# Performance work log

Hardware: AMD Instinct MI355X
Metric: run time of the kernel (lower is better)

Reference implementation:

```python
import jax, jax.numpy as jnp
import numpy as np

N = 32768       # total nodes = NUM_GRAPHS * T
F_IN = 32       # num_features
HC = 64         # hidden_channels
HEADS = 4
E = 524288      # edges before self-loops
NUM_GRAPHS = 64 # == batch.max()+1 by construction
T = 512         # time steps per graph (N // NUM_GRAPHS)
OUT = 24        # output_size
NEG_SLOPE = 0.2 # PyG GATConv default


def gat_layer(x, src, dst, W, a_src, a_dst, b, n_nodes):
    """PyG GATConv (concat=True) with edge softmax over incoming edges."""
    H, C = a_src.shape
    h = (x @ W).reshape(n_nodes, H, C)                    # [N,H,C]
    alpha_src = jnp.sum(h * a_src, axis=-1)               # [N,H]
    alpha_dst = jnp.sum(h * a_dst, axis=-1)               # [N,H]
    e = jax.nn.leaky_relu(alpha_src[src] + alpha_dst[dst], NEG_SLOPE)  # [E,H]
    m = jax.ops.segment_max(e, dst, num_segments=n_nodes)
    e = jnp.exp(e - m[dst])
    s = jax.ops.segment_sum(e, dst, num_segments=n_nodes)
    alpha = e / (s[dst] + 1e-16)                          # [E,H]
    msg = h[src] * alpha[..., None]                       # [E,H,C]
    out = jax.ops.segment_sum(msg, dst, num_segments=n_nodes)  # [N,H,C]
    return out.reshape(n_nodes, H * C) + b


def gru_layer(x, Wih, Whh, bih, bhh):
    """torch nn.GRU single layer, batch_first input x: [B,T,Hin] -> ([B,T,H], h_T)."""
    Bsz = x.shape[0]
    H = Whh.shape[1]

    def step(h, xt):
        gi = xt @ Wih.T + bih
        gh = h @ Whh.T + bhh
        ir, iz, inn = jnp.split(gi, 3, axis=-1)
        hr, hz, hn = jnp.split(gh, 3, axis=-1)
        r = jax.nn.sigmoid(ir + hr)
        z = jax.nn.sigmoid(iz + hz)
        n = jnp.tanh(inn + r * hn)
        h_new = (1.0 - z) * n + z * h
        return h_new, h_new

    h0 = jnp.zeros((Bsz, H), x.dtype)
    hT, ys = jax.lax.scan(step, h0, jnp.swapaxes(x, 0, 1))
    return jnp.swapaxes(ys, 0, 1), hT


def setup_inputs() -> dict:
    key = jax.random.key(0)
    ks = jax.random.split(key, 24)
    sc = 0.1
    inp = {
        "x": jax.random.normal(ks[0], (N, F_IN), dtype=jnp.float32),
        "edge_index": jax.random.randint(ks[1], (2, E), 0, N, dtype=jnp.int32),
        "batch": jnp.repeat(jnp.arange(NUM_GRAPHS, dtype=jnp.int32), T),
        # GAT layer 1: F_IN -> HC x HEADS (concat)
        "W1": sc * jax.random.normal(ks[2], (F_IN, HEADS * HC), dtype=jnp.float32),
        "a_src1": sc * jax.random.normal(ks[3], (HEADS, HC), dtype=jnp.float32),
        "a_dst1": sc * jax.random.normal(ks[4], (HEADS, HC), dtype=jnp.float32),
        "b1": jnp.zeros((HEADS * HC,), dtype=jnp.float32),
        # GAT layer 2: HEADS*HC -> HC, 1 head
        "W2": sc * jax.random.normal(ks[5], (HEADS * HC, HC), dtype=jnp.float32),
        "a_src2": sc * jax.random.normal(ks[6], (1, HC), dtype=jnp.float32),
        "a_dst2": sc * jax.random.normal(ks[7], (1, HC), dtype=jnp.float32),
        "b2": jnp.zeros((HC,), dtype=jnp.float32),
        # GRU (2 layers, input_size == hidden_size == HC)
        "gru_Wih0": sc * jax.random.normal(ks[8], (3 * HC, HC), dtype=jnp.float32),
        "gru_Whh0": sc * jax.random.normal(ks[9], (3 * HC, HC), dtype=jnp.float32),
        "gru_bih0": jnp.zeros((3 * HC,), dtype=jnp.float32),
        "gru_bhh0": jnp.zeros((3 * HC,), dtype=jnp.float32),
        "gru_Wih1": sc * jax.random.normal(ks[10], (3 * HC, HC), dtype=jnp.float32),
        "gru_Whh1": sc * jax.random.normal(ks[11], (3 * HC, HC), dtype=jnp.float32),
        "gru_bih1": jnp.zeros((3 * HC,), dtype=jnp.float32),
        "gru_bhh1": jnp.zeros((3 * HC,), dtype=jnp.float32),
        # Linear head
        "Wl": sc * jax.random.normal(ks[12], (OUT, HC), dtype=jnp.float32),
        "bl": jnp.zeros((OUT,), dtype=jnp.float32),
    }
    return inp


def reference(x, edge_index, batch, W1, a_src1, a_dst1, b1, W2, a_src2, a_dst2, b2,
              gru_Wih0, gru_Whh0, gru_bih0, gru_bhh0,
              gru_Wih1, gru_Whh1, gru_bih1, gru_bhh1, Wl, bl):
    # PyG GATConv default add_self_loops=True
    loops = jnp.arange(N, dtype=edge_index.dtype)
    src = jnp.concatenate([edge_index[0], loops])
    dst = jnp.concatenate([edge_index[1], loops])

    h = jax.nn.elu(gat_layer(x, src, dst, W1, a_src1, a_dst1, b1, N))   # [N, HEADS*HC]
    h = jax.nn.elu(gat_layer(h, src, dst, W2, a_src2, a_dst2, b2, N))   # [N, HC]

    # batch is repeat(arange(NUM_GRAPHS), T) so batch.max()+1 == NUM_GRAPHS (static)
    seq = h.reshape(NUM_GRAPHS, T, HC)
    seq, _ = gru_layer(seq, gru_Wih0, gru_Whh0, gru_bih0, gru_bhh0)
    _, hT = gru_layer(seq, gru_Wih1, gru_Whh1, gru_bih1, gru_bhh1)      # [B, HC]
    return hT @ Wl.T + bl                                               # [B, OUT]
```

## Files before the change

kernel.cpp:

```cpp
#include <hip/hip_runtime.h>
#include <hip/hip_bf16.h>

#define N_NODES 32768
#define F_IN    32
#define HC      64
#define HEADS   4
#define NE      524288
#define NET     (NE + N_NODES)
#define NG      64
#define TT      512
#define OUTF    24

__device__ __forceinline__ float lrelu(float x){ return x > 0.f ? x : 0.2f*x; }
__device__ __forceinline__ float eluf (float x){ return x > 0.f ? x : __expf(x)-1.f; }
__device__ __forceinline__ float sigmf(float x){ return 1.f/(1.f+__expf(-x)); }
__device__ __forceinline__ float tanhfast(float x){ return 1.f - 2.f/(__expf(2.f*x)+1.f); }

__global__ __launch_bounds__(256) void k_deg(const int* __restrict__ ei,
                                             int* __restrict__ deg){
  int e = blockIdx.x*256 + threadIdx.x;
  int d = (e < NE) ? ei[NE+e] : (e - NE);
  atomicAdd(deg + d, 1);
}

__global__ __launch_bounds__(1024) void k_scan(const int* __restrict__ deg,
                                               int* __restrict__ rowptr){
  __shared__ int ps[1024];
  const int t = threadIdx.x;
  const int base = t*32;
  int local[32]; int s = 0;
  #pragma unroll
  for(int i=0;i<32;i++){ local[i]=deg[base+i]; s+=local[i]; }
  ps[t]=s; __syncthreads();
  for(int off=1; off<1024; off<<=1){
    int v = (t>=off) ? ps[t-off] : 0;
    __syncthreads();
    ps[t]+=v;
    __syncthreads();
  }
  int run = (t==0) ? 0 : ps[t-1];
  #pragma unroll
  for(int i=0;i<32;i++){ rowptr[base+i]=run; run+=local[i]; }
  if(t==1023) rowptr[N_NODES]=run;
}

__global__ __launch_bounds__(256) void k_fill(const int* __restrict__ ei,
                                              const int* __restrict__ rowptr,
                                              int* __restrict__ cur,
                                              int* __restrict__ col){
  int e = blockIdx.x*256 + threadIdx.x;
  int s, d;
  if(e < NE){ s = ei[e]; d = ei[NE+e]; } else { s = e-NE; d = s; }
  int pos = atomicAdd(cur + d, 1);
  col[rowptr[d] + pos] = s;
}

__global__ __launch_bounds__(256) void k_gemm1(const float* __restrict__ x,
                                               const float* __restrict__ W1,
                                               float* __restrict__ h1){
  __shared__ __align__(16) float xs[64*32];
  __shared__ __align__(16) float ws[32*256];
  const int tid = threadIdx.x;
  const int row0 = blockIdx.x*64;
  const float4* xg = (const float4*)(x + row0*F_IN);
  float4* xs4 = (float4*)xs;
  for(int i=tid;i<512;i+=256) xs4[i]=xg[i];
  const float4* wg=(const float4*)W1; float4* ws4=(float4*)ws;
  for(int i=tid;i<2048;i+=256) ws4[i]=wg[i];
  __syncthreads();
  float wc[32];
  #pragma unroll
  for(int k=0;k<32;k++) wc[k]=ws[k*256+tid];
  for(int r=0;r<64;r++){
    const float4* xr=(const float4*)(xs + r*32);
    float acc=0.f;
    #pragma unroll
    for(int k4=0;k4<8;k4++){
      float4 v=xr[k4];
      acc += v.x*wc[4*k4]+v.y*wc[4*k4+1]+v.z*wc[4*k4+2]+v.w*wc[4*k4+3];
    }
    h1[(row0+r)*256+tid]=acc;
  }
}

__global__ __launch_bounds__(256) void k_alpha1(const float* __restrict__ h1,
                                                const float* __restrict__ a_src,
                                                const float* __restrict__ a_dst,
                                                float* __restrict__ as1,
                                                float* __restrict__ ad1){
  int t = blockIdx.x*256 + threadIdx.x;
  int n = t>>2, h = t&3;
  const float4* hp=(const float4*)(h1 + n*256 + h*64);
  const float4* ap=(const float4*)(a_src + h*64);
  const float4* dp=(const float4*)(a_dst + h*64);
  float sa=0.f, sd=0.f;
  #pragma unroll
  for(int i=0;i<16;i++){
    float4 v=hp[i], a=ap[i], d=dp[i];
    sa += v.x*a.x+v.y*a.y+v.z*a.z+v.w*a.w;
    sd += v.x*d.x+v.y*d.y+v.z*d.z+v.w*d.w;
  }
  as1[t]=sa; ad1[t]=sd;
}

__global__ __launch_bounds__(256) void k_gat1(const int* __restrict__ rowptr,
                                              const int* __restrict__ col,
                                              const float* __restrict__ as1,
                                              const float* __restrict__ ad1,
                                              const float* __restrict__ h1,
                                              const float* __restrict__ b1,
                                              float* __restrict__ out1){
  const int node = blockIdx.x*4 + (threadIdx.x>>6);
  const int lane = threadIdx.x & 63;
  const int h    = lane>>4;
  const int beg = rowptr[node], end = rowptr[node+1];
  const float ad = ad1[node*4+h];
  float4 acc = make_float4(0.f,0.f,0.f,0.f);
  float s = 0.f;
  int j = beg;
  for(; j+1 < end; j += 2){
    int s0 = col[j], s1 = col[j+1];
    float w0 = __expf(lrelu(as1[s0*4+h] + ad));
    float w1 = __expf(lrelu(as1[s1*4+h] + ad));
    float4 v0 = *(const float4*)(h1 + s0*256 + lane*4);
    float4 v1 = *(const float4*)(h1 + s1*256 + lane*4);
    acc.x += w0*v0.x + w1*v1.x;
    acc.y += w0*v0.y + w1*v1.y;
    acc.z += w0*v0.z + w1*v1.z;
    acc.w += w0*v0.w + w1*v1.w;
    s += w0 + w1;
  }
  if(j < end){
    int s0 = col[j];
    float w0 = __expf(lrelu(as1[s0*4+h] + ad));
    float4 v0 = *(const float4*)(h1 + s0*256 + lane*4);
    acc.x += w0*v0.x; acc.y += w0*v0.y; acc.z += w0*v0.z; acc.w += w0*v0.w;
    s += w0;
  }
  const float inv = 1.f/(s + 1e-16f);
  float4 bb = ((const float4*)b1)[lane];
  float4 o;
  o.x = eluf(acc.x*inv + bb.x);
  o.y = eluf(acc.y*inv + bb.y);
  o.z = eluf(acc.z*inv + bb.z);
  o.w = eluf(acc.w*inv + bb.w);
  ((float4*)(out1 + node*256))[lane] = o;
}

__global__ __launch_bounds__(256) void k_gemm2(const float* __restrict__ in,
                                               const float* __restrict__ W2,
                                               float* __restrict__ h2){
  __shared__ __align__(16) float xs[64*256];
  const int tid=threadIdx.x;
  const int row0=blockIdx.x*64;
  const float4* xg=(const float4*)(in + row0*256);
  float4* xs4=(float4*)xs;
  for(int i=tid;i<4096;i+=256) xs4[i]=xg[i];
  __syncthreads();
  const int c0=(tid&15)*4;
  const int r0=(tid>>4)*4;
  float acc[4][4]={};
  for(int k=0;k<256;k+=4){
    float wv[4][4];
    #pragma unroll
    for(int i=0;i<4;i++){
      float4 w=*(const float4*)(W2+(k+i)*64+c0);
      wv[i][0]=w.x; wv[i][1]=w.y; wv[i][2]=w.z; wv[i][3]=w.w;
    }
    #pragma unroll
    for(int i=0;i<4;i++){
      float4 xv=*(const float4*)(xs+(r0+i)*256+k);
      #pragma unroll
      for(int j=0;j<4;j++)
        acc[i][j]+=xv.x*wv[0][j]+xv.y*wv[1][j]+xv.z*wv[2][j]+xv.w*wv[3][j];
    }
  }
  #pragma unroll
  for(int i=0;i<4;i++)
    *(float4*)(h2+(row0+r0+i)*64+c0)=make_float4(acc[i][0],acc[i][1],acc[i][2],acc[i][3]);
}

__global__ __launch_bounds__(256) void k_alpha2(const float* __restrict__ h2,
                                                const float* __restrict__ a_src,
                                                const float* __restrict__ a_dst,
                                                float* __restrict__ as2,
                                                float* __restrict__ ad2){
  int n = blockIdx.x*256 + threadIdx.x;
  const float4* hp=(const float4*)(h2+n*64);
  float sa=0.f, sd=0.f;
  #pragma unroll
  for(int i=0;i<16;i++){
    float4 v=hp[i];
    float4 a=((const float4*)a_src)[i];
    float4 d=((const float4*)a_dst)[i];
    sa+=v.x*a.x+v.y*a.y+v.z*a.z+v.w*a.w;
    sd+=v.x*d.x+v.y*d.y+v.z*d.z+v.w*d.w;
  }
  as2[n]=sa; ad2[n]=sd;
}

__global__ __launch_bounds__(256) void k_gat2(const int* __restrict__ rowptr,
                                              const int* __restrict__ col,
                                              const float* __restrict__ as2,
                                              const float* __restrict__ ad2,
                                              const float* __restrict__ h2,
                                              const float* __restrict__ b2,
                                              float* __restrict__ out2){
  const int node = blockIdx.x*4 + (threadIdx.x>>6);
  const int lane = threadIdx.x & 63;
  const int beg = rowptr[node], end = rowptr[node+1];
  const float ad = ad2[node];
  float acc = 0.f, s = 0.f;
  int j = beg;
  for(; j+1 < end; j += 2){
    int s0 = col[j], s1 = col[j+1];
    float w0 = __expf(lrelu(as2[s0] + ad));
    float w1 = __expf(lrelu(as2[s1] + ad));
    acc += w0*h2[s0*64+lane] + w1*h2[s1*64+lane];
    s += w0 + w1;
  }
  if(j < end){
    int s0 = col[j];
    float w0 = __expf(lrelu(as2[s0] + ad));
    acc += w0*h2[s0*64+lane];
    s += w0;
  }
  const float inv = 1.f/(s + 1e-16f);
  out2[node*64+lane] = eluf(acc*inv + b2[lane]);
}

__global__ __launch_bounds__(256) void k_gemm_gi(const float* __restrict__ in,
                                                 const float* __restrict__ Wih,
                                                 const float* __restrict__ bih,
                                                 float* __restrict__ gi){
  __shared__ __align__(16) float xs[64*64];
  __shared__ float wT[64*192];
  const int tid=threadIdx.x;
  const int row0=blockIdx.x*64;
  const float4* xg=(const float4*)(in+row0*64);
  float4* xs4=(float4*)xs;
  for(int i=tid;i<1024;i+=256) xs4[i]=xg[i];
  for(int i=tid;i<12288;i+=256){ wT[(i&63)*192+(i>>6)] = Wih[i]; }
  __syncthreads();
  if(tid<192){
    float wr[64];
    #pragma unroll
    for(int k=0;k<64;k++) wr[k]=wT[k*192+tid];
    const float bj=bih[tid];
    for(int r=0;r<64;r++){
      float acc=bj;
      const float4* xr=(const float4*)(xs+r*64);
      #pragma unroll
      for(int k4=0;k4<16;k4++){
        float4 v=xr[k4];
        acc+=v.x*wr[4*k4]+v.y*wr[4*k4+1]+v.z*wr[4*k4+2]+v.w*wr[4*k4+3];
      }
      gi[(row0+r)*192+tid]=acc;
    }
  }
}

__global__ __launch_bounds__(576) void k_gru2(const float* __restrict__ gi1,
                                              const float* __restrict__ Whh0,
                                              const float* __restrict__ bhh0,
                                              const float* __restrict__ Wih1,
                                              const float* __restrict__ bih1,
                                              const float* __restrict__ Whh1,
                                              const float* __restrict__ bhh1,
                                              const float* __restrict__ Wl,
                                              const float* __restrict__ bl,
                                              float* __restrict__ fout){
  __shared__ __align__(16) float h1s[64];
  __shared__ __align__(16) float h2s[64];
  __shared__ float gis1[192];
  __shared__ float gh1s[192];
  __shared__ float gi2s[192];
  __shared__ float gh2s[192];
  const int tid = threadIdx.x;
  const int b   = blockIdx.x;

  const float* Wsel; float bsel; int g;
  if(tid < 192){ g = tid;     Wsel = Whh0; bsel = bhh0[g]; }
  else if(tid < 384){ g = tid-192; Wsel = Wih1; bsel = bih1[g]; }
  else{ g = tid-384; Wsel = Whh1; bsel = bhh1[g]; }
  float wr[64];
  {
    const float4* wp = (const float4*)(Wsel + g*64);
    #pragma unroll
    for(int k4=0;k4<16;k4++){
      float4 w = wp[k4];
      wr[4*k4]=w.x; wr[4*k4+1]=w.y; wr[4*k4+2]=w.z; wr[4*k4+3]=w.w;
    }
  }
  if(tid < 64){ h1s[tid]=0.f; h2s[tid]=0.f; }
  __syncthreads();

  const float* gib = gi1 + (size_t)b*TT*192;
  float giv = (tid < 192) ? gib[tid] : 0.f;

  for(int i=0;i<=TT;i++){
    if(tid < 192){
      if(i < TT){
        gis1[tid] = giv;
        if(i+1 < TT) giv = gib[(i+1)*192 + tid];
        float a0=0.f,a1=0.f,a2=0.f,a3=0.f;
        #pragma unroll
        for(int k4=0;k4<16;k4++){
          float4 h4 = *(const float4*)(h1s + 4*k4);
          a0 += h4.x*wr[4*k4];   a1 += h4.y*wr[4*k4+1];
          a2 += h4.z*wr[4*k4+2]; a3 += h4.w*wr[4*k4+3];
        }
        gh1s[tid] = bsel + ((a0+a1)+(a2+a3));
      }
    } else if(tid < 384){
      if(i >= 1){
        float a0=0.f,a1=0.f,a2=0.f,a3=0.f;
        #pragma unroll
        for(int k4=0;k4<16;k4++){
          float4 h4 = *(const float4*)(h1s + 4*k4);
          a0 += h4.x*wr[4*k4];   a1 += h4.y*wr[4*k4+1];
          a2 += h4.z*wr[4*k4+2]; a3 += h4.w*wr[4*k4+3];
        }
        gi2s[g] = bsel + ((a0+a1)+(a2+a3));
      }
    } else {
      if(i >= 1){
        float a0=0.f,a1=0.f,a2=0.f,a3=0.f;
        #pragma unroll
        for(int k4=0;k4<16;k4++){
          float4 h4 = *(const float4*)(h2s + 4*k4);
          a0 += h4.x*wr[4*k4];   a1 += h4.y*wr[4*k4+1];
          a2 += h4.z*wr[4*k4+2]; a3 += h4.w*wr[4*k4+3];
        }
        gh2s[g] = bsel + ((a0+a1)+(a2+a3));
      }
    }
    __syncthreads();
    if(tid < 64){
      if(i < TT){
        float r = sigmf(gis1[tid]     + gh1s[tid]);
        float z = sigmf(gis1[64+tid]  + gh1s[64+tid]);
        float n = tanhfast(gis1[128+tid] + r*gh1s[128+tid]);
        h1s[tid] = (1.f-z)*n + z*h1s[tid];
      }
    } else if(tid < 128){
      if(i >= 1){
        int c = tid-64;
        float r = sigmf(gi2s[c]     + gh2s[c]);
        float z = sigmf(gi2s[64+c]  + gh2s[64+c]);
        float n = tanhfast(gi2s[128+c] + r*gh2s[128+c]);
        h2s[c] = (1.f-z)*n + z*h2s[c];
      }
    }
    __syncthreads();
  }

  if(tid < 24){
    float acc = bl[tid];
    const float4* wl4 = (const float4*)(Wl + tid*64);
    #pragma unroll
    for(int k4=0;k4<16;k4++){
      float4 h4 = *(const float4*)(h2s + 4*k4);
      float4 w4 = wl4[k4];
      acc += h4.x*w4.x + h4.y*w4.y + h4.z*w4.z + h4.w*w4.w;
    }
    fout[b*24+tid] = acc;
  }
}

extern "C" void kernel_launch(void* const* d_in, const int* in_sizes, int n_in,
                              void* d_out, int out_size, void* d_ws, size_t ws_size,
                              hipStream_t stream){
  const float* x     =(const float*)d_in[0];
  const int*   ei    =(const int*  )d_in[1];
  const float* W1    =(const float*)d_in[3];
  const float* a_src1=(const float*)d_in[4];
  const float* a_dst1=(const float*)d_in[5];
  const float* b1    =(const float*)d_in[6];
  const float* W2    =(const float*)d_in[7];
  const float* a_src2=(const float*)d_in[8];
  const float* a_dst2=(const float*)d_in[9];
  const float* b2    =(const float*)d_in[10];
  const float* Wih0  =(const float*)d_in[11];
  const float* Whh0  =(const float*)d_in[12];
  const float* bih0  =(const float*)d_in[13];
  const float* bhh0  =(const float*)d_in[14];
  const float* Wih1  =(const float*)d_in[15];
  const float* Whh1  =(const float*)d_in[16];
  const float* bih1  =(const float*)d_in[17];
  const float* bhh1  =(const float*)d_in[18];
  const float* Wl    =(const float*)d_in[19];
  const float* bl    =(const float*)d_in[20];

  float* ws   = (float*)d_ws;
  float* h1   = ws;
  float* gi   = ws;
  float* out1 = ws + 8388608;
  float* out2 = out1;
  float* h2   = ws + 16777216;
  float* as1  = ws + 18874368;
  float* ad1  = as1 + 131072;
  float* as2  = ad1 + 131072;
  float* ad2  = as2 + 32768;
  int* rowptr = (int*)(ad2 + 32768);
  int* deg    = rowptr + 32800;
  int* cur    = deg + 32768;
  int* col    = cur + 32768;
  float* fo   = (float*)d_out;

  hipMemsetAsync(deg, 0, 2*32768*sizeof(int), stream);

  k_deg  <<<2176,256,0,stream>>>(ei,deg);
  k_scan <<<1  ,1024,0,stream>>>(deg,rowptr);
  k_fill <<<2176,256,0,stream>>>(ei,rowptr,cur,col);

  k_gemm1 <<<512 ,256,0,stream>>>(x,W1,h1);
  k_alpha1<<<512 ,256,0,stream>>>(h1,a_src1,a_dst1,as1,ad1);
  k_gat1  <<<8192,256,0,stream>>>(rowptr,col,as1,ad1,h1,b1,out1);
  k_gemm2 <<<512 ,256,0,stream>>>(out1,W2,h2);
  k_alpha2<<<128 ,256,0,stream>>>(h2,a_src2,a_dst2,as2,ad2);
  k_gat2  <<<8192,256,0,stream>>>(rowptr,col,as2,ad2,h2,b2,out2);
  k_gemm_gi<<<512,256,0,stream>>>(out2,Wih0,bih0,gi);
  k_gru2  <<<64 ,576,0,stream>>>(gi,Whh0,bhh0,Wih1,bih1,Whh1,bhh1,Wl,bl,fo);
  (void)in_sizes; (void)n_in; (void)out_size; (void)ws_size;
}
```

Before: 875.1 us.

## Restructure GRU kernel into wavefront-specialized pipeline with readlane broadcasts

Replaces the 576-thread two-barrier GRU kernel with a 256-thread kernel where each wavefront owns one role: layer-0 recurrence, layer-1 input projection, layer-1 recurrence, and a prefetcher for the gi stream. Each lane keeps three weight rows in registers and broadcasts the hidden state with readlane instead of reading it from shared memory, and the gate math is fused into the same wavefront. The stages are skewed by one step so each iteration needs only one barrier. The cost is much higher register pressure (192 weight floats per lane) and a two-step pipeline fill.

New measurement: 850.5 us. 1.03x faster.

```diff
diff --git a/kernel.cpp b/kernel.cpp
--- a/kernel.cpp
+++ b/kernel.cpp
@@ -15,6 +15,9 @@
 __device__ __forceinline__ float eluf (float x){ return x > 0.f ? x : __expf(x)-1.f; }
 __device__ __forceinline__ float sigmf(float x){ return 1.f/(1.f+__expf(-x)); }
 __device__ __forceinline__ float tanhfast(float x){ return 1.f - 2.f/(__expf(2.f*x)+1.f); }
+__device__ __forceinline__ float bcast(float v, int k){
+  return __int_as_float(__builtin_amdgcn_readlane(__float_as_int(v), k));
+}
 
 __global__ __launch_bounds__(256) void k_deg(const int* __restrict__ ei,
                                              int* __restrict__ deg){
@@ -260,107 +263,125 @@
   }
 }
 
-__global__ __launch_bounds__(576) void k_gru2(const float* __restrict__ gi1,
-                                              const float* __restrict__ Whh0,
-                                              const float* __restrict__ bhh0,
-                                              const float* __restrict__ Wih1,
-                                              const float* __restrict__ bih1,
-                                              const float* __restrict__ Whh1,
-                                              const float* __restrict__ bhh1,
-                                              const float* __restrict__ Wl,
-                                              const float* __restrict__ bl,
-                                              float* __restrict__ fout){
-  __shared__ __align__(16) float h1s[64];
-  __shared__ __align__(16) float h2s[64];
-  __shared__ float gis1[192];
-  __shared__ float gh1s[192];
-  __shared__ float gi2s[192];
-  __shared__ float gh2s[192];
-  const int tid = threadIdx.x;
-  const int b   = blockIdx.x;
-
-  const float* Wsel; float bsel; int g;
-  if(tid < 192){ g = tid;     Wsel = Whh0; bsel = bhh0[g]; }
-  else if(tid < 384){ g = tid-192; Wsel = Wih1; bsel = bih1[g]; }
-  else{ g = tid-384; Wsel = Whh1; bsel = bhh1[g]; }
-  float wr[64];
+__global__ __launch_bounds__(256,1) void k_gru_pipe(const float* __restrict__ gi1,
+                                                    const float* __restrict__ Whh0,
+                                                    const float* __restrict__ bhh0,
+                                                    const float* __restrict__ Wih1,
+                                                    const float* __restrict__ bih1,
+                                                    const float* __restrict__ Whh1,
+                                                    const float* __restrict__ bhh1,
+                                                    const float* __restrict__ Wl,
+                                                    const float* __restrict__ bl,
+                                                    float* __restrict__ fout){
+  __shared__ float h1s[2][64];
+  __shared__ float gi2s[2][192];
+  __shared__ float gi1b[4][192];
+  __shared__ float h2fin[64];
+  const int tid  = threadIdx.x;
+  const int w    = tid >> 6;
+  const int lane = tid & 63;
+  const int b    = blockIdx.x;
+  const float* gib = gi1 + (size_t)b*TT*192;
+
+  float w0[64], w1[64], w2[64];
+  float b0=0.f, b1=0.f, b2=0.f;
   {
-    const float4* wp = (const float4*)(Wsel + g*64);
-    #pragma unroll
-    for(int k4=0;k4<16;k4++){
-      float4 w = wp[k4];
-      wr[4*k4]=w.x; wr[4*k4+1]=w.y; wr[4*k4+2]=w.z; wr[4*k4+3]=w.w;
-    }
-  }
-  if(tid < 64){ h1s[tid]=0.f; h2s[tid]=0.f; }
+    const float* Wsel = (w==0)?Whh0 : (w==1)?Whh1 : Wih1;
+    const float* bsel = (w==0)?bhh0 : (w==1)?bhh1 : bih1;
+    if(w < 3){
+      const float4* r0 = (const float4*)(Wsel + lane*64);
+      const float4* r1 = (const float4*)(Wsel + (64+lane)*64);
+      const float4* r2 = (const float4*)(Wsel + (128+lane)*64);
+      #pragma unroll
+      for(int k4=0;k4<16;k4++){
+        float4 a=r0[k4], c=r1[k4], d=r2[k4];
+        w0[4*k4]=a.x; w0[4*k4+1]=a.y; w0[4*k4+2]=a.z; w0[4*k4+3]=a.w;
+        w1[4*k4]=c.x; w1[4*k4+1]=c.y; w1[4*k4+2]=c.z; w1[4*k4+3]=c.w;
+        w2[4*k4]=d.x; w2[4*k4+1]=d.y; w2[4*k4+2]=d.z; w2[4*k4+3]=d.w;
+      }
+      b0=bsel[lane]; b1=bsel[64+lane]; b2=bsel[128+lane];
+    } else {
+      #pragma unroll
+      for(int s=0;s<2;s++){
+        float v0=gib[s*192+lane], v1=gib[s*192+64+lane], v2=gib[s*192+128+lane];
+        gi1b[s][lane]=v0; gi1b[s][64+lane]=v1; gi1b[s][128+lane]=v2;
+      }
+    }
+  }
+  float h1r = 0.f, h2r = 0.f;
   __syncthreads();
 
-  const float* gib = gi1 + (size_t)b*TT*192;
-  float giv = (tid < 192) ? gib[tid] : 0.f;
-
-  for(int i=0;i<=TT;i++){
-    if(tid < 192){
+  for(int i=0;i<TT+2;i++){
+    if(w == 0){
       if(i < TT){
-        gis1[tid] = giv;
-        if(i+1 < TT) giv = gib[(i+1)*192 + tid];
-        float a0=0.f,a1=0.f,a2=0.f,a3=0.f;
+        float gr = gi1b[i&3][lane];
+        float gz = gi1b[i&3][64+lane];
+        float gn = gi1b[i&3][128+lane];
+        float a0=b0, a1=b1, a2=b2;
         #pragma unroll
-        for(int k4=0;k4<16;k4++){
-          float4 h4 = *(const float4*)(h1s + 4*k4);
-          a0 += h4.x*wr[4*k4];   a1 += h4.y*wr[4*k4+1];
-          a2 += h4.z*wr[4*k4+2]; a3 += h4.w*wr[4*k4+3];
+        for(int k=0;k<64;k++){
+          float hk = bcast(h1r, k);
+          a0 = fmaf(hk, w0[k], a0);
+          a1 = fmaf(hk, w1[k], a1);
+          a2 = fmaf(hk, w2[k], a2);
         }
-        gh1s[tid] = bsel + ((a0+a1)+(a2+a3));
-      }
-    } else if(tid < 384){
-      if(i >= 1){
-        float a0=0.f,a1=0.f,a2=0.f,a3=0.f;
+        float r = sigmf(gr + a0);
+        float z = sigmf(gz + a1);
+        float n = tanhfast(gn + r*a2);
+        h1r = (1.f-z)*n + z*h1r;
+        h1s[i&1][lane] = h1r;
+      }
+    } else if(w == 2){
+      if(i >= 1 && i <= TT){
+        float h1v = h1s[(i-1)&1][lane];
+        float a0=b0, a1=b1, a2=b2;
         #pragma unroll
-        for(int k4=0;k4<16;k4++){
-          float4 h4 = *(const float4*)(h1s + 4*k4);
-          a0 += h4.x*wr[4*k4];   a1 += h4.y*wr[4*k4+1];
-          a2 += h4.z*wr[4*k4+2]; a3 += h4.w*wr[4*k4+3];
+        for(int k=0;k<64;k++){
+          float hk = bcast(h1v, k);
+          a0 = fmaf(hk, w0[k], a0);
+          a1 = fmaf(hk, w1[k], a1);
+          a2 = fmaf(hk, w2[k], a2);
         }
-        gi2s[g] = bsel + ((a0+a1)+(a2+a3));
+        gi2s[(i-1)&1][lane]     = a0;
+        gi2s[(i-1)&1][64+lane]  = a1;
+        gi2s[(i-1)&1][128+lane] = a2;
+      }
+    } else if(w == 1){
+      if(i >= 2){
+        float gr = gi2s[i&1][lane];
+        float gz = gi2s[i&1][64+lane];
+        float gn = gi2s[i&1][128+lane];
+        float a0=b0, a1=b1, a2=b2;
+        #pragma unroll
+        for(int k=0;k<64;k++){
+          float hk = bcast(h2r, k);
+          a0 = fmaf(hk, w0[k], a0);
+          a1 = fmaf(hk, w1[k], a1);
+          a2 = fmaf(hk, w2[k], a2);
+        }
+        float r = sigmf(gr + a0);
+        float z = sigmf(gz + a1);
+        float n = tanhfast(gn + r*a2);
+        h2r = (1.f-z)*n + z*h2r;
       }
     } else {
-      if(i >= 1){
-        float a0=0.f,a1=0.f,a2=0.f,a3=0.f;
-        #pragma unroll
-        for(int k4=0;k4<16;k4++){
-          float4 h4 = *(const float4*)(h2s + 4*k4);
-          a0 += h4.x*wr[4*k4];   a1 += h4.y*wr[4*k4+1];
-          a2 += h4.z*wr[4*k4+2]; a3 += h4.w*wr[4*k4+3];
-        }
-        gh2s[g] = bsel + ((a0+a1)+(a2+a3));
+      int st = i+2;
+      if(st < TT){
+        float v0=gib[st*192+lane], v1=gib[st*192+64+lane], v2=gib[st*192+128+lane];
+        gi1b[st&3][lane]=v0; gi1b[st&3][64+lane]=v1; gi1b[st&3][128+lane]=v2;
       }
     }
     __syncthreads();
-    if(tid < 64){
-      if(i < TT){
-        float r = sigmf(gis1[tid]     + gh1s[tid]);
-        float z = sigmf(gis1[64+tid]  + gh1s[64+tid]);
-        float n = tanhfast(gis1[128+tid] + r*gh1s[128+tid]);
-        h1s[tid] = (1.f-z)*n + z*h1s[tid];
-      }
-    } else if(tid < 128){
-      if(i >= 1){
-        int c = tid-64;
-        float r = sigmf(gi2s[c]     + gh2s[c]);
-        float z = sigmf(gi2s[64+c]  + gh2s[64+c]);
-        float n = tanhfast(gi2s[128+c] + r*gh2s[128+c]);
-        h2s[c] = (1.f-z)*n + z*h2s[c];
-      }
-    }
-    __syncthreads();
-  }
-
+  }
+
+  if(w == 1) h2fin[lane] = h2r;
+  __syncthreads();
   if(tid < 24){
     float acc = bl[tid];
     const float4* wl4 = (const float4*)(Wl + tid*64);
     #pragma unroll
     for(int k4=0;k4<16;k4++){
-      float4 h4 = *(const float4*)(h2s + 4*k4);
+      float4 h4 = *(const float4*)(h2fin + 4*k4);
       float4 w4 = wl4[k4];
       acc += h4.x*w4.x + h4.y*w4.y + h4.z*w4.z + h4.w*w4.w;
     }
@@ -421,6 +442,6 @@
   k_alpha2<<<128 ,256,0,stream>>>(h2,a_src2,a_dst2,as2,ad2);
   k_gat2  <<<8192,256,0,stream>>>(rowptr,col,as2,ad2,h2,b2,out2);
   k_gemm_gi<<<512,256,0,stream>>>(out2,Wih0,bih0,gi);
-  k_gru2  <<<64 ,576,0,stream>>>(gi,Whh0,bhh0,Wih1,bih1,Whh1,bhh1,Wl,bl,fo);
+  k_gru_pipe<<<64,256,0,stream>>>(gi,Whh0,bhh0,Wih1,bih1,Whh1,bhh1,Wl,bl,fo);
   (void)in_sizes; (void)n_in; (void)out_size; (void)ws_size;
 }
```

## Restructure GRU kernel into wave crews with readlane broadcast and prefetch wave

Applied to the files above, without the earlier changes.

The fused two-layer GRU kernel is reorganised into ten 64-lane waves. Nine waves compute the three recurrent matvecs, taking h from a per-lane register broadcast via readlane instead of float4 LDS reads. A tenth wave double-buffers the next timestep's input gates into shared memory. The gate updates for the two layers are moved onto separate waves (9 and 7). This aims to shorten the serial per-step critical path in the latency-bound recurrence, at the cost of one extra wave and 64 serial readlane+FMA steps per matvec.

New measurement: 979.0 us. 11.9% more time.

```diff
diff --git a/kernel.cpp b/kernel.cpp
--- a/kernel.cpp
+++ b/kernel.cpp
@@ -15,6 +15,9 @@
 __device__ __forceinline__ float eluf (float x){ return x > 0.f ? x : __expf(x)-1.f; }
 __device__ __forceinline__ float sigmf(float x){ return 1.f/(1.f+__expf(-x)); }
 __device__ __forceinline__ float tanhfast(float x){ return 1.f - 2.f/(__expf(2.f*x)+1.f); }
+__device__ __forceinline__ float bcast(float v, int k){
+  return __int_as_float(__builtin_amdgcn_readlane(__float_as_int(v), k));
+}
 
 __global__ __launch_bounds__(256) void k_deg(const int* __restrict__ ei,
                                              int* __restrict__ deg){
@@ -260,96 +263,84 @@
   }
 }
 
-__global__ __launch_bounds__(576) void k_gru2(const float* __restrict__ gi1,
-                                              const float* __restrict__ Whh0,
-                                              const float* __restrict__ bhh0,
-                                              const float* __restrict__ Wih1,
-                                              const float* __restrict__ bih1,
-                                              const float* __restrict__ Whh1,
-                                              const float* __restrict__ bhh1,
-                                              const float* __restrict__ Wl,
-                                              const float* __restrict__ bl,
-                                              float* __restrict__ fout){
-  __shared__ __align__(16) float h1s[64];
-  __shared__ __align__(16) float h2s[64];
-  __shared__ float gis1[192];
+__global__ __launch_bounds__(640,1) void k_gru9(const float* __restrict__ gi1,
+                                                const float* __restrict__ Whh0,
+                                                const float* __restrict__ bhh0,
+                                                const float* __restrict__ Wih1,
+                                                const float* __restrict__ bih1,
+                                                const float* __restrict__ Whh1,
+                                                const float* __restrict__ bhh1,
+                                                const float* __restrict__ Wl,
+                                                const float* __restrict__ bl,
+                                                float* __restrict__ fout){
+  __shared__ float h1s[64];
+  __shared__ float h2s[64];
   __shared__ float gh1s[192];
   __shared__ float gi2s[192];
   __shared__ float gh2s[192];
-  const int tid = threadIdx.x;
-  const int b   = blockIdx.x;
-
-  const float* Wsel; float bsel; int g;
-  if(tid < 192){ g = tid;     Wsel = Whh0; bsel = bhh0[g]; }
-  else if(tid < 384){ g = tid-192; Wsel = Wih1; bsel = bih1[g]; }
-  else{ g = tid-384; Wsel = Whh1; bsel = bhh1[g]; }
+  __shared__ float g1r[2][192];
+  const int tid  = threadIdx.x;
+  const int w    = tid >> 6;
+  const int lane = tid & 63;
+  const int b    = blockIdx.x;
+  const float* gib = gi1 + (size_t)b*TT*192;
+
   float wr[64];
-  {
-    const float4* wp = (const float4*)(Wsel + g*64);
+  float bias = 0.f;
+  int   crew = 0, row = 0;
+  float* dst = gh1s;
+  if(w < 9){
+    crew = w / 3;
+    row  = (w % 3)*64 + lane;
+    const float* W  = (crew==0) ? Whh0 : (crew==1) ? Wih1 : Whh1;
+    const float* bb = (crew==0) ? bhh0 : (crew==1) ? bih1 : bhh1;
+    dst = (crew==0) ? gh1s : (crew==1) ? gi2s : gh2s;
+    const float4* wp = (const float4*)(W + row*64);
     #pragma unroll
     for(int k4=0;k4<16;k4++){
-      float4 w = wp[k4];
-      wr[4*k4]=w.x; wr[4*k4+1]=w.y; wr[4*k4+2]=w.z; wr[4*k4+3]=w.w;
-    }
+      float4 v = wp[k4];
+      wr[4*k4]=v.x; wr[4*k4+1]=v.y; wr[4*k4+2]=v.z; wr[4*k4+3]=v.w;
+    }
+    bias = bb[row];
+  } else {
+    g1r[0][lane]     = gib[lane];
+    g1r[0][64+lane]  = gib[64+lane];
+    g1r[0][128+lane] = gib[128+lane];
   }
   if(tid < 64){ h1s[tid]=0.f; h2s[tid]=0.f; }
   __syncthreads();
 
-  const float* gib = gi1 + (size_t)b*TT*192;
-  float giv = (tid < 192) ? gib[tid] : 0.f;
-
   for(int i=0;i<=TT;i++){
-    if(tid < 192){
-      if(i < TT){
-        gis1[tid] = giv;
-        if(i+1 < TT) giv = gib[(i+1)*192 + tid];
-        float a0=0.f,a1=0.f,a2=0.f,a3=0.f;
+    if(w < 9){
+      bool act = (crew==0) ? (i < TT) : (i >= 1);
+      if(act){
+        float hv = (crew==2) ? h2s[lane] : h1s[lane];
+        float acc = bias;
         #pragma unroll
-        for(int k4=0;k4<16;k4++){
-          float4 h4 = *(const float4*)(h1s + 4*k4);
-          a0 += h4.x*wr[4*k4];   a1 += h4.y*wr[4*k4+1];
-          a2 += h4.z*wr[4*k4+2]; a3 += h4.w*wr[4*k4+3];
-        }
-        gh1s[tid] = bsel + ((a0+a1)+(a2+a3));
-      }
-    } else if(tid < 384){
-      if(i >= 1){
-        float a0=0.f,a1=0.f,a2=0.f,a3=0.f;
-        #pragma unroll
-        for(int k4=0;k4<16;k4++){
-          float4 h4 = *(const float4*)(h1s + 4*k4);
-          a0 += h4.x*wr[4*k4];   a1 += h4.y*wr[4*k4+1];
-          a2 += h4.z*wr[4*k4+2]; a3 += h4.w*wr[4*k4+3];
-        }
-        gi2s[g] = bsel + ((a0+a1)+(a2+a3));
+        for(int k=0;k<64;k++) acc = fmaf(bcast(hv,k), wr[k], acc);
+        dst[row] = acc;
       }
     } else {
+      int st = i+1;
+      if(st < TT){
+        float v0=gib[st*192+lane], v1=gib[st*192+64+lane], v2=gib[st*192+128+lane];
+        g1r[st&1][lane]=v0; g1r[st&1][64+lane]=v1; g1r[st&1][128+lane]=v2;
+      }
+    }
+    __syncthreads();
+    if(w == 9){
+      if(i < TT){
+        float r = sigmf(g1r[i&1][lane]     + gh1s[lane]);
+        float z = sigmf(g1r[i&1][64+lane]  + gh1s[64+lane]);
+        float n = tanhfast(g1r[i&1][128+lane] + r*gh1s[128+lane]);
+        h1s[lane] = (1.f-z)*n + z*h1s[lane];
+      }
+    } else if(w == 7){
       if(i >= 1){
-        float a0=0.f,a1=0.f,a2=0.f,a3=0.f;
-        #pragma unroll
-        for(int k4=0;k4<16;k4++){
-          float4 h4 = *(const float4*)(h2s + 4*k4);
-          a0 += h4.x*wr[4*k4];   a1 += h4.y*wr[4*k4+1];
-          a2 += h4.z*wr[4*k4+2]; a3 += h4.w*wr[4*k4+3];
-        }
-        gh2s[g] = bsel + ((a0+a1)+(a2+a3));
-      }
-    }
-    __syncthreads();
-    if(tid < 64){
-      if(i < TT){
-        float r = sigmf(gis1[tid]     + gh1s[tid]);
-        float z = sigmf(gis1[64+tid]  + gh1s[64+tid]);
-        float n = tanhfast(gis1[128+tid] + r*gh1s[128+tid]);
-        h1s[tid] = (1.f-z)*n + z*h1s[tid];
-      }
-    } else if(tid < 128){
-      if(i >= 1){
-        int c = tid-64;
-        float r = sigmf(gi2s[c]     + gh2s[c]);
-        float z = sigmf(gi2s[64+c]  + gh2s[64+c]);
-        float n = tanhfast(gi2s[128+c] + r*gh2s[128+c]);
-        h2s[c] = (1.f-z)*n + z*h2s[c];
+        float r = sigmf(gi2s[lane]     + gh2s[lane]);
+        float z = sigmf(gi2s[64+lane]  + gh2s[64+lane]);
+        float n = tanhfast(gi2s[128+lane] + r*gh2s[128+lane]);
+        h2s[lane] = (1.f-z)*n + z*h2s[lane];
       }
     }
     __syncthreads();
@@ -421,6 +412,6 @@
   k_alpha2<<<128 ,256,0,stream>>>(h2,a_src2,a_dst2,as2,ad2);
   k_gat2  <<<8192,256,0,stream>>>(rowptr,col,as2,ad2,h2,b2,out2);
   k_gemm_gi<<<512,256,0,stream>>>(out2,Wih0,bih0,gi);
-  k_gru2  <<<64 ,576,0,stream>>>(gi,Whh0,bhh0,Wih1,bih1,Whh1,bhh1,Wl,bl,fo);
+  k_gru9  <<<64 ,640,0,stream>>>(gi,Whh0,bhh0,Wih1,bih1,Whh1,bhh1,Wl,bl,fo);
   (void)in_sizes; (void)n_in; (void)out_size; (void)ws_size;
 }
```
